# Kernel tuning notes

Measured on AMD Instinct MI355X. Metric: run time of the kernel, lower is better.

## Reference

```python
import jax, jax.numpy as jnp
import numpy as np

N = 100000   # nodes
E = 1000000  # edges
G = 5000     # graphs
IN = 64; H = 64; ED = 16; OUT = 1
NUM_LAYERS = 3; NUM_TIMESTEPS = 2
SLOPE = 0.01

if NUM_LAYERS >= NUM_TIMESTEPS:
    CACHED_INDEX = list(range(-NUM_TIMESTEPS, 0))
else:
    CACHED_INDEX = list(range(-NUM_LAYERS, 0)) + [-1] * (NUM_TIMESTEPS - NUM_LAYERS)


def leaky(x):
    return jnp.where(x > 0, x, SLOPE * x)


def seg_softmax(scores, index, num_segments):
    # scores: [E] edge scores, softmax within segments given by index (PyG softmax, +1e-16 denom)
    m = jax.ops.segment_max(scores, index, num_segments)
    m = jnp.where(jnp.isfinite(m), m, 0.0)
    e = jnp.exp(scores - m[index])
    s = jax.ops.segment_sum(e, index, num_segments)
    return e / (s[index] + 1e-16)


def gru_cell(x, h, wih, whh, bih, bhh):
    # torch.nn.GRUCell math
    gi = x @ wih.T + bih
    gh = h @ whh.T + bhh
    ir, iz, inn = jnp.split(gi, 3, axis=-1)
    hr, hz, hn = jnp.split(gh, 3, axis=-1)
    r = jax.nn.sigmoid(ir + hr)
    z = jax.nn.sigmoid(iz + hz)
    n = jnp.tanh(inn + r * hn)
    return (1.0 - z) * n + z * h


def setup_inputs() -> dict:
    key = jax.random.key(0)
    ks = jax.random.split(key, 32)
    f32 = jnp.float32
    def w(k, shape, fan_in):
        return jax.random.normal(k, shape, f32) * (1.0 / np.sqrt(fan_in))
    L2 = NUM_LAYERS - 1
    inp = {}
    inp['raw'] = jax.random.normal(ks[0], (N, IN), f32)
    inp['edge_index'] = jax.random.randint(ks[1], (2, E), 0, N)
    inp['edge_attr'] = jax.random.normal(ks[2], (E, ED), f32)
    inp['batch'] = jnp.sort(jax.random.randint(ks[3], (N,), 0, G))
    inp['lin1_w'] = w(ks[4], (H, IN), IN); inp['lin1_b'] = jnp.zeros((H,), f32)
    inp['gate_nl_w'] = w(ks[5], (H, IN + ED), IN + ED); inp['gate_nl_b'] = jnp.zeros((H,), f32)
    inp['gate_align_w'] = w(ks[6], (1, 2 * H), 2 * H); inp['gate_align_b'] = jnp.zeros((1,), f32)
    inp['gate_attend_w'] = w(ks[7], (H, H), H); inp['gate_attend_b'] = jnp.zeros((H,), f32)
    inp['conv_align_w'] = w(ks[8], (L2, 1, 2 * H), 2 * H); inp['conv_align_b'] = jnp.zeros((L2, 1), f32)
    inp['conv_attend_w'] = w(ks[9], (L2, H, H), H); inp['conv_attend_b'] = jnp.zeros((L2, H), f32)
    inp['atom_gru_wih'] = w(ks[10], (NUM_LAYERS, 3 * H, H), H)
    inp['atom_gru_whh'] = w(ks[11], (NUM_LAYERS, 3 * H, H), H)
    inp['atom_gru_bih'] = jnp.zeros((NUM_LAYERS, 3 * H), f32)
    inp['atom_gru_bhh'] = jnp.zeros((NUM_LAYERS, 3 * H), f32)
    inp['mol_align_w'] = w(ks[12], (1, 2 * H), 2 * H); inp['mol_align_b'] = jnp.zeros((1,), f32)
    inp['mol_attend_w'] = w(ks[13], (H, H), H); inp['mol_attend_b'] = jnp.zeros((H,), f32)
    inp['mol_gru_wih'] = w(ks[14], (3 * H, H), H)
    inp['mol_gru_whh'] = w(ks[15], (3 * H, H), H)
    inp['mol_gru_bih'] = jnp.zeros((3 * H,), f32)
    inp['mol_gru_bhh'] = jnp.zeros((3 * H,), f32)
    inp['lin2_w'] = w(ks[16], (OUT, H), H); inp['lin2_b'] = jnp.zeros((OUT,), f32)
    return inp


def reference(raw, edge_index, edge_attr, batch,
              lin1_w, lin1_b,
              gate_nl_w, gate_nl_b, gate_align_w, gate_align_b, gate_attend_w, gate_attend_b,
              conv_align_w, conv_align_b, conv_attend_w, conv_attend_b,
              atom_gru_wih, atom_gru_whh, atom_gru_bih, atom_gru_bhh,
              mol_align_w, mol_align_b, mol_attend_w, mol_attend_b,
              mol_gru_wih, mol_gru_whh, mol_gru_bih, mol_gru_bhh,
              lin2_w, lin2_b):
    src, dst = edge_index[0], edge_index[1]
    x = leaky(raw @ lin1_w.T + lin1_b)  # [N, H]

    # --- GATEConv (layer 0): x_j from raw, x_i from x ---
    xj = leaky(jnp.concatenate([raw[src], edge_attr], axis=-1) @ gate_nl_w.T + gate_nl_b)  # [E, H]
    score = leaky(jnp.concatenate([x[dst], xj], axis=-1) @ gate_align_w.T + gate_align_b)  # [E, 1]
    aw = seg_softmax(score[:, 0], dst, N)[:, None]
    msg = (xj @ gate_attend_w.T + gate_attend_b) * aw
    h = jax.nn.elu(jax.ops.segment_sum(msg, dst, N))
    x = jax.nn.relu(gru_cell(h, x, atom_gru_wih[0], atom_gru_whh[0], atom_gru_bih[0], atom_gru_bhh[0]))
    cached = [x]

    # --- GATConv layers 1..L-1 ---
    for l in range(NUM_LAYERS - 1):
        xi, xj = x[dst], x[src]
        score = leaky(jnp.concatenate([xi, xj], axis=-1) @ conv_align_w[l].T + conv_align_b[l])
        aw = seg_softmax(score[:, 0], dst, N)[:, None]
        msg = (xj @ conv_attend_w[l].T + conv_attend_b[l]) * aw
        h = jax.nn.elu(jax.ops.segment_sum(msg, dst, N))
        x = jax.nn.relu(gru_cell(h, x, atom_gru_wih[l + 1], atom_gru_whh[l + 1],
                                 atom_gru_bih[l + 1], atom_gru_bhh[l + 1]))
        cached.append(x)

    # --- molecule-level readout ---
    out = jax.nn.relu(jax.ops.segment_sum(x, batch, G))  # [G, H]
    for t in range(NUM_TIMESTEPS):
        mixed = (x + cached[CACHED_INDEX[t]]) * 0.5  # [N, H] (x_j); x_i = out[batch]
        score = leaky(jnp.concatenate([out[batch], mixed], axis=-1) @ mol_align_w.T + mol_align_b)
        aw = seg_softmax(score[:, 0], batch, G)[:, None]
        msg = (mixed @ mol_attend_w.T + mol_attend_b) * aw
        h = jax.nn.elu(jax.ops.segment_sum(msg, batch, G))
        out = jax.nn.relu(gru_cell(h, out, mol_gru_wih, mol_gru_whh, mol_gru_bih, mol_gru_bhh))

    return out @ lin2_w.T + lin2_b  # [G, OUT]
```

## Files before the change

kernel.cpp:

```cpp
#include <hip/hip_runtime.h>
#include <math.h>

#define NPAD 65

__device__ __forceinline__ float leaky(float x) { return x > 0.f ? x : 0.01f * x; }
__device__ __forceinline__ float eluf(float x)  { return x > 0.f ? x : (__expf(x) - 1.f); }
__device__ __forceinline__ float sigm(float x)  { return 1.f / (1.f + __expf(-x)); }
__device__ __forceinline__ float tanhfast(float x) { return 1.f - 2.f / (__expf(2.f * x) + 1.f); }

__device__ __forceinline__ float bcastf(float v, int k) {
    return __uint_as_float((unsigned)__builtin_amdgcn_readlane((int)__float_as_uint(v), k));
}
__device__ __forceinline__ int bcasti(int v, int k) {
    return __builtin_amdgcn_readlane(v, k);
}
__device__ __forceinline__ float wredsum(float v) {
    #pragma unroll
    for (int off = 32; off; off >>= 1) v += __shfl_xor(v, off);
    return v;
}
__device__ __forceinline__ float wredmax(float v) {
    #pragma unroll
    for (int off = 32; off; off >>= 1) v = fmaxf(v, __shfl_xor(v, off));
    return v;
}

__global__ __launch_bounds__(256) void k_hist(const int* __restrict__ ei, int* __restrict__ deg, int E_) {
    int e = blockIdx.x * 256 + threadIdx.x;
    if (e < E_) atomicAdd(&deg[ei[E_ + e]], 1);
}

__global__ __launch_bounds__(256) void k_scan1(const int* __restrict__ deg, int* __restrict__ bsum, int N_) {
    __shared__ int s[256];
    int i = blockIdx.x * 256 + threadIdx.x;
    s[threadIdx.x] = (i < N_) ? deg[i] : 0;
    __syncthreads();
    for (int off = 128; off; off >>= 1) {
        if (threadIdx.x < off) s[threadIdx.x] += s[threadIdx.x + off];
        __syncthreads();
    }
    if (threadIdx.x == 0) bsum[blockIdx.x] = s[0];
}

__global__ __launch_bounds__(512) void k_scan2(int* __restrict__ bsum, int nb) {
    __shared__ int s[512];
    __shared__ int carry_s;
    if (threadIdx.x == 0) carry_s = 0;
    __syncthreads();
    for (int base = 0; base < nb; base += 512) {
        int t = threadIdx.x;
        int idx = base + t;
        int v = (idx < nb) ? bsum[idx] : 0;
        s[t] = v;
        __syncthreads();
        #pragma unroll
        for (int off = 1; off < 512; off <<= 1) {
            int u = (t >= off) ? s[t - off] : 0;
            __syncthreads();
            s[t] += u;
            __syncthreads();
        }
        int carry = carry_s;
        if (idx < nb) bsum[idx] = carry + s[t] - v;
        __syncthreads();
        if (t == 0) carry_s = carry + s[511];
        __syncthreads();
    }
}

__global__ __launch_bounds__(256) void k_scan3(const int* __restrict__ deg, const int* __restrict__ bsum,
                                               int* __restrict__ row, int* __restrict__ cur, int N_, int E_) {
    __shared__ int s[256];
    int i = blockIdx.x * 256 + threadIdx.x;
    int d = (i < N_) ? deg[i] : 0;
    s[threadIdx.x] = d;
    __syncthreads();
    for (int off = 1; off < 256; off <<= 1) {
        int v = (threadIdx.x >= off) ? s[threadIdx.x - off] : 0;
        __syncthreads();
        s[threadIdx.x] += v;
        __syncthreads();
    }
    if (i < N_) {
        int ex = bsum[blockIdx.x] + s[threadIdx.x] - d;
        row[i] = ex; cur[i] = ex;
    }
    if (i == N_ - 1) row[N_] = E_;
}

__global__ __launch_bounds__(256) void k_scatter(const int* __restrict__ ei, int* __restrict__ cur,
                                                 int* __restrict__ csrc, int* __restrict__ ceid, int E_) {
    int e = blockIdx.x * 256 + threadIdx.x;
    if (e >= E_) return;
    int dst = ei[E_ + e];
    int slot = atomicAdd(&cur[dst], 1);
    csrc[slot] = ei[e];
    ceid[slot] = e;
}

__global__ __launch_bounds__(256) void k_gbounds(const int* __restrict__ batch, int* __restrict__ gst,
                                                 int N_, int G_) {
    int i = blockIdx.x * 256 + threadIdx.x;
    if (i >= N_) return;
    int b = batch[i];
    int prev = (i == 0) ? -1 : batch[i - 1];
    for (int g = prev + 1; g <= b; ++g) gst[g] = i;
    if (i == N_ - 1) { for (int g = b + 1; g <= G_; ++g) gst[g] = N_; }
}

__global__ __launch_bounds__(256) void k_dense64(
    const float* __restrict__ in, const float* __restrict__ w, int wstride,
    const float* __restrict__ b, float* __restrict__ outp, int M, int act,
    const float* __restrict__ dva, float* __restrict__ dsout)
{
    __shared__ float ti[64 * NPAD];
    __shared__ float to[64 * NPAD];
    int r0 = blockIdx.x * 64;
    for (int i = threadIdx.x; i < 4096; i += 256) {
        int r = i >> 6, c = i & 63; int gr = r0 + r;
        ti[r * NPAD + c] = (gr < M) ? in[(size_t)gr * 64 + c] : 0.f;
    }
    __syncthreads();
    int n = threadIdx.x & 63;
    int jl = __builtin_amdgcn_readfirstlane((threadIdx.x >> 6) << 4);
    float acc[16];
    #pragma unroll
    for (int jj = 0; jj < 16; ++jj) acc[jj] = b[jl + jj];
    for (int kc = 0; kc < 64; kc += 16) {
        float xr[16];
        #pragma unroll
        for (int i = 0; i < 16; ++i) xr[i] = ti[n * NPAD + kc + i];
        #pragma unroll
        for (int jj = 0; jj < 16; ++jj) {
            const float* wr = w + (jl + jj) * wstride + kc;
            #pragma unroll
            for (int i = 0; i < 16; ++i) acc[jj] = fmaf(wr[i], xr[i], acc[jj]);
        }
    }
    #pragma unroll
    for (int jj = 0; jj < 16; ++jj) {
        float v = acc[jj];
        to[n * NPAD + jl + jj] = act ? leaky(v) : v;
    }
    __syncthreads();
    for (int i = threadIdx.x; i < 4096; i += 256) {
        int r = i >> 6, c = i & 63; int gr = r0 + r;
        if (gr < M) outp[(size_t)gr * 64 + c] = to[r * NPAD + c];
    }
    if (dsout != nullptr) {
        int wv = threadIdx.x >> 6;
        float wval = dva[n];
        #pragma unroll 4
        for (int q = 0; q < 16; ++q) {
            int r = (wv << 4) + q; int gr = r0 + r;
            float pv = wredsum(to[r * NPAD + n] * wval);
            if (n == 0 && gr < M) dsout[gr] = pv;
        }
    }
}

#define GDOT(acc, A0, A1, A2, A3) \
    acc = fmaf(A0.x, w2[0], acc);  acc = fmaf(A0.y, w2[1], acc);  \
    acc = fmaf(A0.z, w2[2], acc);  acc = fmaf(A0.w, w2[3], acc);  \
    acc = fmaf(A1.x, w2[4], acc);  acc = fmaf(A1.y, w2[5], acc);  \
    acc = fmaf(A1.z, w2[6], acc);  acc = fmaf(A1.w, w2[7], acc);  \
    acc = fmaf(A2.x, w2[8], acc);  acc = fmaf(A2.y, w2[9], acc);  \
    acc = fmaf(A2.z, w2[10], acc); acc = fmaf(A2.w, w2[11], acc); \
    acc = fmaf(A3.x, w2[12], acc); acc = fmaf(A3.y, w2[13], acc); \
    acc = fmaf(A3.z, w2[14], acc); acc = fmaf(A3.w, w2[15], acc);

__global__ __launch_bounds__(256, 4) void k_gate_gather(
    const float* __restrict__ u, const float* __restrict__ ea,
    const int* __restrict__ row, const int* __restrict__ csrc, const int* __restrict__ ceid,
    const float* __restrict__ wnl,
    const float* __restrict__ gaw, const float* __restrict__ gab,
    const float* __restrict__ sarr, float* __restrict__ Agg, int N_)
{
    int wid = (blockIdx.x * 256 + threadIdx.x) >> 6;
    int lane = threadIdx.x & 63;
    if (wid >= N_) return;
    float w2[16];
    #pragma unroll
    for (int k = 0; k < 16; ++k) w2[k] = wnl[lane * 80 + 64 + k];
    float g2 = gaw[64 + lane];
    float gb = gab[0];
    float sdst = sarr[wid];
    int beg = row[wid], end = row[wid + 1];
    float m = -INFINITY, d = 0.f, S = 0.f;
    for (int cs = beg; cs < end; cs += 64) {
        int cnt = min(64, end - cs);
        int src_l = 0, eid_l = 0;
        if (lane < cnt) { src_l = csrc[cs + lane]; eid_l = ceid[cs + lane]; }
        int cnt2 = (cnt + 1) & ~1;
        int j1 = (1 < cnt) ? 1 : 0;
        int s0 = bcasti(src_l, 0), s1 = bcasti(src_l, j1);
        int e0 = bcasti(eid_l, 0), e1 = bcasti(eid_l, j1);
        float u0 = u[(size_t)s0 * 64 + lane];
        float u1 = u[(size_t)s1 * 64 + lane];
        const float4* p0 = (const float4*)(ea + (size_t)e0 * 16);
        const float4* p1 = (const float4*)(ea + (size_t)e1 * 16);
        float4 a00 = p0[0], a01 = p0[1], a02 = p0[2], a03 = p0[3];
        float4 a10 = p1[0], a11 = p1[1], a12 = p1[2], a13 = p1[3];
        for (int l = 0; l < cnt2; l += 2) {
            int ln0 = (l + 2 < cnt) ? l + 2 : l;
            int ln1 = (l + 3 < cnt) ? l + 3 : l;
            int ns0 = bcasti(src_l, ln0), ns1 = bcasti(src_l, ln1);
            int ne0 = bcasti(eid_l, ln0), ne1 = bcasti(eid_l, ln1);
            float nu0 = u[(size_t)ns0 * 64 + lane];
            float nu1 = u[(size_t)ns1 * 64 + lane];
            const float4* q0 = (const float4*)(ea + (size_t)ne0 * 16);
            const float4* q1 = (const float4*)(ea + (size_t)ne1 * 16);
            float4 b00 = q0[0], b01 = q0[1], b02 = q0[2], b03 = q0[3];
            float4 b10 = q1[0], b11 = q1[1], b12 = q1[2], b13 = q1[3];
            float acc0 = u0, acc1 = u1;
            GDOT(acc0, a00, a01, a02, a03)
            GDOT(acc1, a10, a11, a12, a13)
            float xj0 = leaky(acc0), xj1 = leaky(acc1);
            float t0 = xj0 * g2, t1 = xj1 * g2;
            #pragma unroll
            for (int off = 32; off; off >>= 1) {
                t0 += __shfl_xor(t0, off);
                t1 += __shfl_xor(t1, off);
            }
            float sc0 = leaky(sdst + t0 + gb);
            float sc1 = (l + 1 < cnt) ? leaky(sdst + t1 + gb) : -INFINITY;
            float mn = fmaxf(m, fmaxf(sc0, sc1));
            float c = __expf(m - mn);
            float q0e = __expf(sc0 - mn), q1e = __expf(sc1 - mn);
            S = S * c;
            S = fmaf(q0e, xj0, S); S = fmaf(q1e, xj1, S);
            d = d * c + (q0e + q1e);
            m = mn;
            u0 = nu0; u1 = nu1;
            a00 = b00; a01 = b01; a02 = b02; a03 = b03;
            a10 = b10; a11 = b11; a12 = b12; a13 = b13;
        }
    }
    Agg[(size_t)wid * 64 + lane] = S / (d + 1e-16f);
}

__global__ __launch_bounds__(256) void k_gat_gather(
    const int* __restrict__ row, const int* __restrict__ csrc,
    const float* __restrict__ x, const float* __restrict__ sarr,
    const float* __restrict__ tarr, const float* __restrict__ cb,
    float* __restrict__ Agg, int N_)
{
    int wid = (blockIdx.x * 256 + threadIdx.x) >> 6;
    int lane = threadIdx.x & 63;
    if (wid >= N_) return;
    float sdst = sarr[wid];
    float cbv = cb[0];
    int beg = row[wid], end = row[wid + 1];
    float m = -INFINITY, d = 0.f, S = 0.f;
    for (int cs = beg; cs < end; cs += 64) {
        int cnt = min(64, end - cs);
        int src_l = 0;
        if (lane < cnt) src_l = csrc[cs + lane];
        int s0 = bcasti(src_l, 0), s1 = bcasti(src_l, 1);
        int s2 = bcasti(src_l, 2), s3 = bcasti(src_l, 3);
        float r0 = x[(size_t)s0 * 64 + lane];
        float r1 = x[(size_t)s1 * 64 + lane];
        float r2 = x[(size_t)s2 * 64 + lane];
        float r3 = x[(size_t)s3 * 64 + lane];
        float sc_l = -INFINITY;
        if (lane < cnt) sc_l = leaky(sdst + tarr[src_l] + cbv);
        float cmax = wredmax(sc_l);
        float mn = fmaxf(m, cmax);
        float c = __expf(m - mn);
        float w_l = __expf(sc_l - mn);
        d = d * c + wredsum(w_l);
        S *= c;
        int cnt4 = (cnt + 3) & ~3;
        for (int l = 0; l < cnt4; l += 4) {
            int ln = (l + 4 < cnt4) ? l + 4 : 0;
            int t0 = bcasti(src_l, ln),     t1 = bcasti(src_l, ln + 1);
            int t2 = bcasti(src_l, ln + 2), t3 = bcasti(src_l, ln + 3);
            float p0 = x[(size_t)t0 * 64 + lane];
            float p1 = x[(size_t)t1 * 64 + lane];
            float p2 = x[(size_t)t2 * 64 + lane];
            float p3 = x[(size_t)t3 * 64 + lane];
            float w0 = bcastf(w_l, l),     w1 = bcastf(w_l, l + 1);
            float w2 = bcastf(w_l, l + 2), w3 = bcastf(w_l, l + 3);
            S = fmaf(w0, r0, S); S = fmaf(w1, r1, S);
            S = fmaf(w2, r2, S); S = fmaf(w3, r3, S);
            r0 = p0; r1 = p1; r2 = p2; r3 = p3;
        }
        m = mn;
    }
    Agg[(size_t)wid * 64 + lane] = S / (d + 1e-16f);
}

__global__ __launch_bounds__(512, 4) void k_node_update(
    const float* __restrict__ agg, const float* __restrict__ xold,
    const float* __restrict__ wa, const float* __restrict__ ba,
    const float* __restrict__ wih, const float* __restrict__ whh,
    const float* __restrict__ bih, const float* __restrict__ bhh,
    float* __restrict__ xout, int M,
    const float* __restrict__ dwa, const float* __restrict__ dwb,
    float* __restrict__ sout, float* __restrict__ tout, int mode)
{
    __shared__ float tA[128 * NPAD];
    __shared__ float tX[128 * NPAD];
    int r0 = blockIdx.x * 128;
    for (int j = threadIdx.x; j < 2048; j += 512) {
        int r = j >> 4, c4 = (j & 15) << 2; int gr = r0 + r;
        float4 av = make_float4(0.f, 0.f, 0.f, 0.f), xv = av;
        if (gr < M) {
            av = *(const float4*)(agg  + (size_t)gr * 64 + c4);
            xv = *(const float4*)(xold + (size_t)gr * 64 + c4);
        }
        int b = r * NPAD + c4;
        tA[b] = av.x; tA[b + 1] = av.y; tA[b + 2] = av.z; tA[b + 3] = av.w;
        tX[b] = xv.x; tX[b + 1] = xv.y; tX[b + 2] = xv.z; tX[b + 3] = xv.w;
    }
    __syncthreads();
    int n = threadIdx.x & 63;
    int jl = __builtin_amdgcn_readfirstlane((threadIdx.x >> 6) << 3);

    float hvA[8], hvB[8];
    {
        float accA[8], accB[8];
        #pragma unroll
        for (int jj = 0; jj < 8; ++jj) { float bv = ba[jl + jj]; accA[jj] = bv; accB[jj] = bv; }
        for (int kc = 0; kc < 64; kc += 16) {
            float aA[16], aB[16];
            #pragma unroll
            for (int i = 0; i < 16; ++i) {
                aA[i] = tA[n * NPAD + kc + i];
                aB[i] = tA[(n + 64) * NPAD + kc + i];
            }
            #pragma unroll
            for (int jj = 0; jj < 8; ++jj) {
                const float* wr = wa + (jl + jj) * 64 + kc;
                #pragma unroll
                for (int i = 0; i < 16; ++i) {
                    float wv = wr[i];
                    accA[jj] = fmaf(wv, aA[i], accA[jj]);
                    accB[jj] = fmaf(wv, aB[i], accB[jj]);
                }
            }
        }
        #pragma unroll
        for (int jj = 0; jj < 8; ++jj) { hvA[jj] = eluf(accA[jj]); hvB[jj] = eluf(accB[jj]); }
    }
    __syncthreads();
    #pragma unroll
    for (int jj = 0; jj < 8; ++jj) {
        tA[n * NPAD + jl + jj] = hvA[jj];
        tA[(n + 64) * NPAD + jl + jj] = hvB[jj];
    }
    __syncthreads();

    float rAc[8], rBc[8], zAc[8], zBc[8], nAc[8], nBc[8], hAc[8], hBc[8];
    #pragma unroll
    for (int jj = 0; jj < 8; ++jj) {
        float brz = bih[jl + jj] + bhh[jl + jj];
        float bz  = bih[64 + jl + jj] + bhh[64 + jl + jj];
        rAc[jj] = brz; rBc[jj] = brz;
        zAc[jj] = bz;  zBc[jj] = bz;
        nAc[jj] = bih[128 + jl + jj]; nBc[jj] = nAc[jj];
        hAc[jj] = bhh[128 + jl + jj]; hBc[jj] = hAc[jj];
    }
    for (int kc = 0; kc < 64; kc += 8) {
        float h0[8], h1[8], x0[8], x1[8];
        #pragma unroll
        for (int i = 0; i < 8; ++i) {
            h0[i] = tA[n * NPAD + kc + i];
            h1[i] = tA[(n + 64) * NPAD + kc + i];
            x0[i] = tX[n * NPAD + kc + i];
            x1[i] = tX[(n + 64) * NPAD + kc + i];
        }
        #pragma unroll
        for (int jj = 0; jj < 8; ++jj) {
            const float* w1 = wih + (jl + jj) * 64 + kc;
            const float* w4 = whh + (jl + jj) * 64 + kc;
            const float* w2 = wih + (64 + jl + jj) * 64 + kc;
            const float* w5 = whh + (64 + jl + jj) * 64 + kc;
            const float* w3 = wih + (128 + jl + jj) * 64 + kc;
            const float* w6 = whh + (128 + jl + jj) * 64 + kc;
            #pragma unroll
            for (int i = 0; i < 8; ++i) {
                float v1 = w1[i], v4 = w4[i], v2 = w2[i];
                float v5 = w5[i], v3 = w3[i], v6 = w6[i];
                rAc[jj] = fmaf(v1, h0[i], rAc[jj]); rAc[jj] = fmaf(v4, x0[i], rAc[jj]);
                rBc[jj] = fmaf(v1, h1[i], rBc[jj]); rBc[jj] = fmaf(v4, x1[i], rBc[jj]);
                zAc[jj] = fmaf(v2, h0[i], zAc[jj]); zAc[jj] = fmaf(v5, x0[i], zAc[jj]);
                zBc[jj] = fmaf(v2, h1[i], zBc[jj]); zBc[jj] = fmaf(v5, x1[i], zBc[jj]);
                nAc[jj] = fmaf(v3, h0[i], nAc[jj]); hAc[jj] = fmaf(v6, x0[i], hAc[jj]);
                nBc[jj] = fmaf(v3, h1[i], nBc[jj]); hBc[jj] = fmaf(v6, x1[i], hBc[jj]);
            }
        }
    }
    float paA = 0.f, pbA = 0.f, paB = 0.f, pbB = 0.f;
    #pragma unroll
    for (int jj = 0; jj < 8; ++jj) {
        float r = sigm(rAc[jj]);
        float z = sigm(zAc[jj]);
        float nn = tanhfast(nAc[jj] + r * hAc[jj]);
        float xo = tX[n * NPAD + jl + jj];
        float v = (1.f - z) * nn + z * xo;
        hvA[jj] = fmaxf(v, 0.f);

        float rb = sigm(rBc[jj]);
        float zb = sigm(zBc[jj]);
        float nb_ = tanhfast(nBc[jj] + rb * hBc[jj]);
        float xob = tX[(n + 64) * NPAD + jl + jj];
        float vb = (1.f - zb) * nb_ + zb * xob;
        hvB[jj] = fmaxf(vb, 0.f);

        if (sout != nullptr) {
            float wav = dwa[jl + jj];
            float wbv = (mode == 0) ? dwb[jl + jj] : wav;
            float a1A = (mode == 1) ? 0.5f * (hvA[jj] + xo)  : hvA[jj];
            float a1B = (mode == 1) ? 0.5f * (hvB[jj] + xob) : hvB[jj];
            paA = fmaf(a1A, wav, paA); pbA = fmaf(hvA[jj], wbv, pbA);
            paB = fmaf(a1B, wav, paB); pbB = fmaf(hvB[jj], wbv, pbB);
        }
    }
    __syncthreads();
    #pragma unroll
    for (int jj = 0; jj < 8; ++jj) {
        tA[n * NPAD + jl + jj] = hvA[jj];
        tA[(n + 64) * NPAD + jl + jj] = hvB[jj];
    }
    if (sout != nullptr) {
        int w2i = (threadIdx.x >> 6) << 1;
        tX[n * 17 + w2i]            = paA;
        tX[n * 17 + w2i + 1]        = pbA;
        tX[(n + 64) * 17 + w2i]     = paB;
        tX[(n + 64) * 17 + w2i + 1] = pbB;
    }
    __syncthreads();
    for (int j = threadIdx.x; j < 2048; j += 512) {
        int r = j >> 4, c4 = (j & 15) << 2; int gr = r0 + r;
        if (gr < M) {
            int b = r * NPAD + c4;
            float4 ov = make_float4(tA[b], tA[b + 1], tA[b + 2], tA[b + 3]);
            *(float4*)(xout + (size_t)gr * 64 + c4) = ov;
        }
    }
    if (sout != nullptr && threadIdx.x < 128) {
        int r = threadIdx.x; int gr = r0 + r;
        if (gr < M) {
            float sa = 0.f, sb = 0.f;
            #pragma unroll
            for (int w = 0; w < 16; w += 2) { sa += tX[r * 17 + w]; sb += tX[r * 17 + w + 1]; }
            if (mode == 2) {
                sout[gr] = sa + dwb[0];
            } else {
                sout[gr] = sa; tout[gr] = sb;
            }
        }
    }
}

__global__ __launch_bounds__(256) void k_seg_sum_relu(
    const float* __restrict__ x, const int* __restrict__ gst,
    float* __restrict__ outp, int G_)
{
    int g = (blockIdx.x * 256 + threadIdx.x) >> 6;
    int lane = threadIdx.x & 63;
    if (g >= G_) return;
    float S0 = 0.f, S1 = 0.f, S2 = 0.f, S3 = 0.f;
    int end = gst[g + 1];
    int i = gst[g];
    for (; i + 4 <= end; i += 4) {
        S0 += x[(size_t)i * 64 + lane];
        S1 += x[(size_t)(i + 1) * 64 + lane];
        S2 += x[(size_t)(i + 2) * 64 + lane];
        S3 += x[(size_t)(i + 3) * 64 + lane];
    }
    for (; i < end; ++i) S0 += x[(size_t)i * 64 + lane];
    outp[(size_t)g * 64 + lane] = fmaxf((S0 + S1) + (S2 + S3), 0.f);
}

__global__ __launch_bounds__(256) void k_mol_gather(
    const float* __restrict__ xf, const float* __restrict__ cach,
    const float* __restrict__ stateIn, const int* __restrict__ gst,
    const float* __restrict__ dd,
    const float* __restrict__ maw, const float* __restrict__ mab,
    float* __restrict__ Agg, int G_)
{
    int g = (blockIdx.x * 256 + threadIdx.x) >> 6;
    int lane = threadIdx.x & 63;
    if (g >= G_) return;
    float o = stateIn[(size_t)g * 64 + lane];
    float og = wredsum(o * maw[lane]);
    float mb = mab[0];
    int beg = gst[g], end = gst[g + 1];
    float m = -INFINITY, d = 0.f, S = 0.f;
    for (int cs = beg; cs < end; cs += 64) {
        int cnt = min(64, end - cs);
        size_t rb = (size_t)cs * 64 + lane;
        float x0 = xf[rb],      c0 = cach[rb];
        float x1 = xf[rb + 64], c1 = cach[rb + 64];
        float x2 = xf[rb + 128], c2 = cach[rb + 128];
        float x3 = xf[rb + 192], c3 = cach[rb + 192];
        float sc_l = -INFINITY;
        if (lane < cnt) sc_l = leaky(og + dd[cs + lane] + mb);
        float cmax = wredmax(sc_l);
        float mn = fmaxf(m, cmax);
        float c = __expf(m - mn);
        float w_l = __expf(sc_l - mn);
        d = d * c + wredsum(w_l);
        S *= c;
        int cnt4 = (cnt + 3) & ~3;
        for (int l = 0; l < cnt4; l += 4) {
            int ln = (l + 4 < cnt4) ? l + 4 : 0;
            size_t rn = (size_t)(cs + ln) * 64 + lane;
            float y0 = xf[rn],       d0 = cach[rn];
            float y1 = xf[rn + 64],  d1 = cach[rn + 64];
            float y2 = xf[rn + 128], d2 = cach[rn + 128];
            float y3 = xf[rn + 192], d3 = cach[rn + 192];
            float w0 = bcastf(w_l, l),     w1 = bcastf(w_l, l + 1);
            float w2 = bcastf(w_l, l + 2), w3 = bcastf(w_l, l + 3);
            S = fmaf(w0, 0.5f * (x0 + c0), S);
            S = fmaf(w1, 0.5f * (x1 + c1), S);
            S = fmaf(w2, 0.5f * (x2 + c2), S);
            S = fmaf(w3, 0.5f * (x3 + c3), S);
            x0 = y0; c0 = d0; x1 = y1; c1 = d1;
            x2 = y2; c2 = d2; x3 = y3; c3 = d3;
        }
        m = mn;
    }
    Agg[(size_t)g * 64 + lane] = S / (d + 1e-16f);
}

extern "C" void kernel_launch(void* const* d_in, const int* in_sizes, int n_in,
                              void* d_out, int out_size, void* d_ws, size_t ws_size,
                              hipStream_t stream) {
    const float* raw           = (const float*)d_in[0];
    const int*   ei            = (const int*)d_in[1];
    const float* ea            = (const float*)d_in[2];
    const int*   batch         = (const int*)d_in[3];
    const float* lin1_w        = (const float*)d_in[4];
    const float* lin1_b        = (const float*)d_in[5];
    const float* gate_nl_w     = (const float*)d_in[6];
    const float* gate_nl_b     = (const float*)d_in[7];
    const float* gate_align_w  = (const float*)d_in[8];
    const float* gate_align_b  = (const float*)d_in[9];
    const float* gate_attend_w = (const float*)d_in[10];
    const float* gate_attend_b = (const float*)d_in[11];
    const float* conv_align_w  = (const float*)d_in[12];
    const float* conv_align_b  = (const float*)d_in[13];
    const float* conv_attend_w = (const float*)d_in[14];
    const float* conv_attend_b = (const float*)d_in[15];
    const float* gru_wih       = (const float*)d_in[16];
    const float* gru_whh       = (const float*)d_in[17];
    const float* gru_bih       = (const float*)d_in[18];
    const float* gru_bhh       = (const float*)d_in[19];
    const float* mol_align_w   = (const float*)d_in[20];
    const float* mol_align_b   = (const float*)d_in[21];
    const float* mol_attend_w  = (const float*)d_in[22];
    const float* mol_attend_b  = (const float*)d_in[23];
    const float* mol_wih       = (const float*)d_in[24];
    const float* mol_whh       = (const float*)d_in[25];
    const float* mol_bih       = (const float*)d_in[26];
    const float* mol_bhh       = (const float*)d_in[27];
    const float* lin2_w        = (const float*)d_in[28];
    const float* lin2_b        = (const float*)d_in[29];
    float* out = (float*)d_out;

    const int N = in_sizes[3];
    const int E = in_sizes[1] / 2;
    const int G = out_size;
    const size_t N64 = (size_t)N * 64;
    const size_t G64 = (size_t)G * 64;

    float* f = (float*)d_ws;
    float* xA    = f;
    float* xB    = xA + N64;
    float* xD    = xB + N64;
    float* Agg   = xD + N64;
    float* u     = Agg + N64;
    float* sN    = u + N64;
    float* tN    = sN + N;
    float* dd    = tN + N;
    float* outS  = dd + N;
    float* outS2 = outS + G64;
    float* aggG  = outS2 + G64;
    int* row  = (int*)(aggG + G64);
    int* csrc = row + (N + 1);
    int* ceid = csrc + E;
    int* bsum = ceid + E;
    int* gst  = bsum + 512;
    int* deg = (int*)Agg;
    int* cur = deg + N;

    const int nb_node64  = (N + 63) / 64;
    const int nb_node128 = (N + 127) / 128;
    const int nb_edge   = (E + 255) / 256;
    const int nb_nodes  = (N + 255) / 256;
    const int nb_waveN  = (N + 3) / 4;
    const int nb_waveG  = (G + 3) / 4;
    const int nb_nodeG  = (G + 127) / 128;

    hipMemsetAsync(deg, 0, (size_t)N * 4, stream);
    k_hist<<<nb_edge, 256, 0, stream>>>(ei, deg, E);
    k_scan1<<<nb_nodes, 256, 0, stream>>>(deg, bsum, N);
    k_scan2<<<1, 512, 0, stream>>>(bsum, nb_nodes);
    k_scan3<<<nb_nodes, 256, 0, stream>>>(deg, bsum, row, cur, N, E);
    k_scatter<<<nb_edge, 256, 0, stream>>>(ei, cur, csrc, ceid, E);
    k_gbounds<<<nb_nodes, 256, 0, stream>>>(batch, gst, N, G);

    k_dense64<<<nb_node64, 256, 0, stream>>>(raw, lin1_w, 64, lin1_b, xA, N, 1,
                                             gate_align_w, sN);
    k_dense64<<<nb_node64, 256, 0, stream>>>(raw, gate_nl_w, 80, gate_nl_b, u, N, 0,
                                             nullptr, nullptr);

    k_gate_gather<<<nb_waveN, 256, 0, stream>>>(u, ea, row, csrc, ceid,
                                                gate_nl_w, gate_align_w, gate_align_b,
                                                sN, Agg, N);
    k_node_update<<<nb_node128, 512, 0, stream>>>(Agg, xA, gate_attend_w, gate_attend_b,
                                                  gru_wih, gru_whh, gru_bih, gru_bhh, xB, N,
                                                  conv_align_w, conv_align_w + 64, sN, tN, 0);

    k_gat_gather<<<nb_waveN, 256, 0, stream>>>(row, csrc, xB, sN, tN, conv_align_b, Agg, N);
    k_node_update<<<nb_node128, 512, 0, stream>>>(Agg, xB, conv_attend_w, conv_attend_b,
                                                  gru_wih + 12288, gru_whh + 12288,
                                                  gru_bih + 192, gru_bhh + 192, xD, N,
                                                  conv_align_w + 128, conv_align_w + 192, sN, tN, 0);

    k_gat_gather<<<nb_waveN, 256, 0, stream>>>(row, csrc, xD, sN, tN, conv_align_b + 1, Agg, N);
    k_node_update<<<nb_node128, 512, 0, stream>>>(Agg, xD, conv_attend_w + 4096, conv_attend_b + 64,
                                                  gru_wih + 24576, gru_whh + 24576,
                                                  gru_bih + 384, gru_bhh + 384, xA, N,
                                                  mol_align_w + 64, mol_align_w + 64, dd, tN, 1);

    k_seg_sum_relu<<<nb_waveG, 256, 0, stream>>>(xA, gst, outS, G);

    k_mol_gather<<<nb_waveG, 256, 0, stream>>>(xA, xD, outS, gst, dd,
                                               mol_align_w, mol_align_b, aggG, G);
    k_node_update<<<nb_nodeG, 512, 0, stream>>>(aggG, outS, mol_attend_w, mol_attend_b,
                                                mol_wih, mol_whh, mol_bih, mol_bhh, outS2, G,
                                                nullptr, nullptr, nullptr, nullptr, 0);
    k_mol_gather<<<nb_waveG, 256, 0, stream>>>(xA, xA, outS2, gst, tN,
                                               mol_align_w, mol_align_b, aggG, G);
    k_node_update<<<nb_nodeG, 512, 0, stream>>>(aggG, outS2, mol_attend_w, mol_attend_b,
                                                mol_wih, mol_whh, mol_bih, mol_bhh, outS, G,
                                                lin2_w, lin2_b, out, nullptr, 2);
}
```

Baseline: 1.071 ms.

## Fuse dual input projections into one kernel and vectorize LDS tiles with float4

The two dense 64-wide projections of the raw node features (lin1 and the gate_nl input part) are merged into one kernel, so the input tile is loaded once and both outputs are written in a single launch. Shared-memory tiles are padded to 68 floats instead of 65 so rows stay 16-byte aligned, and LDS reads and writes in the dense and node-update kernels become float4 accesses. The readfirstlane hint on the weight-row offset is dropped. The wider padding can bring back LDS bank conflicts on strided row accesses, and the fused kernel holds twice the accumulators, which raises register pressure.

Result: slower. 3.184 ms (+197.2%).

```diff
diff --git a/kernel.cpp b/kernel.cpp
--- a/kernel.cpp
+++ b/kernel.cpp
@@ -2,6 +2,7 @@
 #include <math.h>
 
 #define NPAD 65
+#define NP2  68
 
 __device__ __forceinline__ float leaky(float x) { return x > 0.f ? x : 0.01f * x; }
 __device__ __forceinline__ float eluf(float x)  { return x > 0.f ? x : (__expf(x) - 1.f); }
@@ -108,44 +109,57 @@
     if (i == N_ - 1) { for (int g = b + 1; g <= G_; ++g) gst[g] = N_; }
 }
 
-__global__ __launch_bounds__(256) void k_dense64(
-    const float* __restrict__ in, const float* __restrict__ w, int wstride,
-    const float* __restrict__ b, float* __restrict__ outp, int M, int act,
+__global__ __launch_bounds__(256) void k_dense64_dual(
+    const float* __restrict__ in,
+    const float* __restrict__ w1, const float* __restrict__ b1,
+    const float* __restrict__ w2, const float* __restrict__ b2,
+    float* __restrict__ out1, float* __restrict__ out2, int M,
     const float* __restrict__ dva, float* __restrict__ dsout)
 {
-    __shared__ float ti[64 * NPAD];
-    __shared__ float to[64 * NPAD];
+    __shared__ float ti[64 * NP2];
+    __shared__ float t1[64 * NP2];
+    __shared__ float t2[64 * NP2];
     int r0 = blockIdx.x * 64;
-    for (int i = threadIdx.x; i < 4096; i += 256) {
-        int r = i >> 6, c = i & 63; int gr = r0 + r;
-        ti[r * NPAD + c] = (gr < M) ? in[(size_t)gr * 64 + c] : 0.f;
+    for (int j = threadIdx.x; j < 1024; j += 256) {
+        int r = j >> 4, c4 = (j & 15) << 2; int gr = r0 + r;
+        float4 v = make_float4(0.f, 0.f, 0.f, 0.f);
+        if (gr < M) v = *(const float4*)(in + (size_t)gr * 64 + c4);
+        *(float4*)&ti[r * NP2 + c4] = v;
     }
     __syncthreads();
     int n = threadIdx.x & 63;
-    int jl = __builtin_amdgcn_readfirstlane((threadIdx.x >> 6) << 4);
-    float acc[16];
+    int jl = (threadIdx.x >> 6) << 4;
+    float a1[16], a2[16];
     #pragma unroll
-    for (int jj = 0; jj < 16; ++jj) acc[jj] = b[jl + jj];
+    for (int jj = 0; jj < 16; ++jj) { a1[jj] = b1[jl + jj]; a2[jj] = b2[jl + jj]; }
     for (int kc = 0; kc < 64; kc += 16) {
         float xr[16];
         #pragma unroll
-        for (int i = 0; i < 16; ++i) xr[i] = ti[n * NPAD + kc + i];
+        for (int q = 0; q < 4; ++q)
+            *(float4*)&xr[q << 2] = *(const float4*)&ti[n * NP2 + kc + (q << 2)];
         #pragma unroll
         for (int jj = 0; jj < 16; ++jj) {
-            const float* wr = w + (jl + jj) * wstride + kc;
+            const float* wr1 = w1 + (jl + jj) * 64 + kc;
+            const float* wr2 = w2 + (jl + jj) * 80 + kc;
             #pragma unroll
-            for (int i = 0; i < 16; ++i) acc[jj] = fmaf(wr[i], xr[i], acc[jj]);
+            for (int i = 0; i < 16; ++i) {
+                a1[jj] = fmaf(wr1[i], xr[i], a1[jj]);
+                a2[jj] = fmaf(wr2[i], xr[i], a2[jj]);
+            }
         }
     }
     #pragma unroll
     for (int jj = 0; jj < 16; ++jj) {
-        float v = acc[jj];
-        to[n * NPAD + jl + jj] = act ? leaky(v) : v;
-    }
-    __syncthreads();
-    for (int i = threadIdx.x; i < 4096; i += 256) {
-        int r = i >> 6, c = i & 63; int gr = r0 + r;
-        if (gr < M) outp[(size_t)gr * 64 + c] = to[r * NPAD + c];
+        t1[n * NP2 + jl + jj] = leaky(a1[jj]);
+        t2[n * NP2 + jl + jj] = a2[jj];
+    }
+    __syncthreads();
+    for (int j = threadIdx.x; j < 1024; j += 256) {
+        int r = j >> 4, c4 = (j & 15) << 2; int gr = r0 + r;
+        if (gr < M) {
+            *(float4*)(out1 + (size_t)gr * 64 + c4) = *(const float4*)&t1[r * NP2 + c4];
+            *(float4*)(out2 + (size_t)gr * 64 + c4) = *(const float4*)&t2[r * NP2 + c4];
+        }
     }
     if (dsout != nullptr) {
         int wv = threadIdx.x >> 6;
@@ -153,7 +167,7 @@
         #pragma unroll 4
         for (int q = 0; q < 16; ++q) {
             int r = (wv << 4) + q; int gr = r0 + r;
-            float pv = wredsum(to[r * NPAD + n] * wval);
+            float pv = wredsum(t1[r * NP2 + n] * wval);
             if (n == 0 && gr < M) dsout[gr] = pv;
         }
     }
@@ -299,8 +313,8 @@
     const float* __restrict__ dwa, const float* __restrict__ dwb,
     float* __restrict__ sout, float* __restrict__ tout, int mode)
 {
-    __shared__ float tA[128 * NPAD];
-    __shared__ float tX[128 * NPAD];
+    __shared__ float tA[128 * NP2];
+    __shared__ float tX[128 * NP2];
     int r0 = blockIdx.x * 128;
     for (int j = threadIdx.x; j < 2048; j += 512) {
         int r = j >> 4, c4 = (j & 15) << 2; int gr = r0 + r;
@@ -309,13 +323,12 @@
             av = *(const float4*)(agg  + (size_t)gr * 64 + c4);
             xv = *(const float4*)(xold + (size_t)gr * 64 + c4);
         }
-        int b = r * NPAD + c4;
-        tA[b] = av.x; tA[b + 1] = av.y; tA[b + 2] = av.z; tA[b + 3] = av.w;
-        tX[b] = xv.x; tX[b + 1] = xv.y; tX[b + 2] = xv.z; tX[b + 3] = xv.w;
+        *(float4*)&tA[r * NP2 + c4] = av;
+        *(float4*)&tX[r * NP2 + c4] = xv;
     }
     __syncthreads();
     int n = threadIdx.x & 63;
-    int jl = __builtin_amdgcn_readfirstlane((threadIdx.x >> 6) << 3);
+    int jl = (threadIdx.x >> 6) << 3;
 
     float hvA[8], hvB[8];
     {
@@ -325,9 +338,9 @@
         for (int kc = 0; kc < 64; kc += 16) {
             float aA[16], aB[16];
             #pragma unroll
-            for (int i = 0; i < 16; ++i) {
-                aA[i] = tA[n * NPAD + kc + i];
-                aB[i] = tA[(n + 64) * NPAD + kc + i];
+            for (int q = 0; q < 4; ++q) {
+                *(float4*)&aA[q << 2] = *(const float4*)&tA[n * NP2 + kc + (q << 2)];
+                *(float4*)&aB[q << 2] = *(const float4*)&tA[(n + 64) * NP2 + kc + (q << 2)];
             }
             #pragma unroll
             for (int jj = 0; jj < 8; ++jj) {
@@ -344,11 +357,10 @@
         for (int jj = 0; jj < 8; ++jj) { hvA[jj] = eluf(accA[jj]); hvB[jj] = eluf(accB[jj]); }
     }
     __syncthreads();
-    #pragma unroll
-    for (int jj = 0; jj < 8; ++jj) {
-        tA[n * NPAD + jl + jj] = hvA[jj];
-        tA[(n + 64) * NPAD + jl + jj] = hvB[jj];
-    }
+    *(float4*)&tA[n * NP2 + jl]            = make_float4(hvA[0], hvA[1], hvA[2], hvA[3]);
+    *(float4*)&tA[n * NP2 + jl + 4]        = make_float4(hvA[4], hvA[5], hvA[6], hvA[7]);
+    *(float4*)&tA[(n + 64) * NP2 + jl]     = make_float4(hvB[0], hvB[1], hvB[2], hvB[3]);
+    *(float4*)&tA[(n + 64) * NP2 + jl + 4] = make_float4(hvB[4], hvB[5], hvB[6], hvB[7]);
     __syncthreads();
 
     float rAc[8], rBc[8], zAc[8], zBc[8], nAc[8], nBc[8], hAc[8], hBc[8];
@@ -363,13 +375,14 @@
     }
     for (int kc = 0; kc < 64; kc += 8) {
         float h0[8], h1[8], x0[8], x1[8];
-        #pragma unroll
-        for (int i = 0; i < 8; ++i) {
-            h0[i] = tA[n * NPAD + kc + i];
-            h1[i] = tA[(n + 64) * NPAD + kc + i];
-            x0[i] = tX[n * NPAD + kc + i];
-            x1[i] = tX[(n + 64) * NPAD + kc + i];
-        }
+        *(float4*)&h0[0] = *(const float4*)&tA[n * NP2 + kc];
+        *(float4*)&h0[4] = *(const float4*)&tA[n * NP2 + kc + 4];
+        *(float4*)&h1[0] = *(const float4*)&tA[(n + 64) * NP2 + kc];
+        *(float4*)&h1[4] = *(const float4*)&tA[(n + 64) * NP2 + kc + 4];
+        *(float4*)&x0[0] = *(const float4*)&tX[n * NP2 + kc];
+        *(float4*)&x0[4] = *(const float4*)&tX[n * NP2 + kc + 4];
+        *(float4*)&x1[0] = *(const float4*)&tX[(n + 64) * NP2 + kc];
+        *(float4*)&x1[4] = *(const float4*)&tX[(n + 64) * NP2 + kc + 4];
         #pragma unroll
         for (int jj = 0; jj < 8; ++jj) {
             const float* w1 = wih + (jl + jj) * 64 + kc;
@@ -397,14 +410,14 @@
         float r = sigm(rAc[jj]);
         float z = sigm(zAc[jj]);
         float nn = tanhfast(nAc[jj] + r * hAc[jj]);
-        float xo = tX[n * NPAD + jl + jj];
+        float xo = tX[n * NP2 + jl + jj];
         float v = (1.f - z) * nn + z * xo;
         hvA[jj] = fmaxf(v, 0.f);
 
         float rb = sigm(rBc[jj]);
         float zb = sigm(zBc[jj]);
         float nb_ = tanhfast(nBc[jj] + rb * hBc[jj]);
-        float xob = tX[(n + 64) * NPAD + jl + jj];
+        float xob = tX[(n + 64) * NP2 + jl + jj];
         float vb = (1.f - zb) * nb_ + zb * xob;
         hvB[jj] = fmaxf(vb, 0.f);
 
@@ -418,11 +431,10 @@
         }
     }
     __syncthreads();
-    #pragma unroll
-    for (int jj = 0; jj < 8; ++jj) {
-        tA[n * NPAD + jl + jj] = hvA[jj];
-        tA[(n + 64) * NPAD + jl + jj] = hvB[jj];
-    }
+    *(float4*)&tA[n * NP2 + jl]            = make_float4(hvA[0], hvA[1], hvA[2], hvA[3]);
+    *(float4*)&tA[n * NP2 + jl + 4]        = make_float4(hvA[4], hvA[5], hvA[6], hvA[7]);
+    *(float4*)&tA[(n + 64) * NP2 + jl]     = make_float4(hvB[0], hvB[1], hvB[2], hvB[3]);
+    *(float4*)&tA[(n + 64) * NP2 + jl + 4] = make_float4(hvB[4], hvB[5], hvB[6], hvB[7]);
     if (sout != nullptr) {
         int w2i = (threadIdx.x >> 6) << 1;
         tX[n * 17 + w2i]            = paA;
@@ -434,9 +446,7 @@
     for (int j = threadIdx.x; j < 2048; j += 512) {
         int r = j >> 4, c4 = (j & 15) << 2; int gr = r0 + r;
         if (gr < M) {
-            int b = r * NPAD + c4;
-            float4 ov = make_float4(tA[b], tA[b + 1], tA[b + 2], tA[b + 3]);
-            *(float4*)(xout + (size_t)gr * 64 + c4) = ov;
+            *(float4*)(xout + (size_t)gr * 64 + c4) = *(const float4*)&tA[r * NP2 + c4];
         }
     }
     if (sout != nullptr && threadIdx.x < 128) {
@@ -603,10 +613,9 @@
     k_scatter<<<nb_edge, 256, 0, stream>>>(ei, cur, csrc, ceid, E);
     k_gbounds<<<nb_nodes, 256, 0, stream>>>(batch, gst, N, G);
 
-    k_dense64<<<nb_node64, 256, 0, stream>>>(raw, lin1_w, 64, lin1_b, xA, N, 1,
-                                             gate_align_w, sN);
-    k_dense64<<<nb_node64, 256, 0, stream>>>(raw, gate_nl_w, 80, gate_nl_b, u, N, 0,
-                                             nullptr, nullptr);
+    k_dense64_dual<<<nb_node64, 256, 0, stream>>>(raw, lin1_w, lin1_b,
+                                                  gate_nl_w, gate_nl_b,
+                                                  xA, u, N, gate_align_w, sN);
 
     k_gate_gather<<<nb_waveN, 256, 0, stream>>>(u, ea, row, csrc, ceid,
                                                 gate_nl_w, gate_align_w, gate_align_b,
```
